# Kernel optimization log

Hardware: AMD Instinct MI355X
Metric: run time of the kernel (lower is better)

## Reference

```python
import jax, jax.numpy as jnp
import numpy as np

D_MODEL = 2048
EXPAND = 2
D_INNER = EXPAND * D_MODEL      # 4096
HEADDIM = 64
NHEADS = D_INNER // HEADDIM     # 64
D_STATE = 128
NGROUPS = 1
D_CONV = 4
CHUNK = 256
CONV_DIM = D_INNER + 2 * NGROUPS * D_STATE          # 4352
D_IN_PROJ = 2 * D_INNER + 2 * NGROUPS * D_STATE + NHEADS  # 8512
EPS = 1e-5


def setup_inputs() -> dict:
    key = jax.random.key(0)
    ks = jax.random.split(key, 8)
    B, L = 2, 2048
    u = jax.random.normal(ks[0], (B, L, D_MODEL), jnp.float32)
    W_in = jax.random.normal(ks[1], (D_IN_PROJ, D_MODEL), jnp.float32) / np.sqrt(D_MODEL)
    conv_w = jax.random.normal(ks[2], (CONV_DIM, D_CONV), jnp.float32) * 0.2
    conv_b = jax.random.normal(ks[3], (CONV_DIM,), jnp.float32) * 0.05
    # dt_bias initialized exactly as in the torch module
    dt = jnp.exp(jax.random.uniform(ks[4], (NHEADS,)) * (np.log(0.1) - np.log(0.001)) + np.log(0.001))
    dt = jnp.clip(dt, 1e-4)
    dt_bias = dt + jnp.log(-jnp.expm1(-dt))
    A_log = jnp.log(jax.random.uniform(ks[5], (NHEADS,), minval=1.0, maxval=16.0))
    D = jnp.ones((NHEADS,), jnp.float32)
    norm_w = jnp.ones((D_INNER,), jnp.float32)
    W_out = jax.random.normal(ks[6], (D_MODEL, D_INNER), jnp.float32) / np.sqrt(D_INNER)
    return dict(u=u, W_in=W_in, conv_w=conv_w, conv_b=conv_b, dt_bias=dt_bias,
                A_log=A_log, D=D, norm_w=norm_w, W_out=W_out)


def _segsum(x):
    # x: (..., l) -> (..., l, l) with out[i, j] = sum_{k=j+1..i} x[k] (lower-tri, -inf above)
    cs = jnp.cumsum(x, -1)
    seg = cs[..., :, None] - cs[..., None, :]
    l = x.shape[-1]
    mask = jnp.tril(jnp.ones((l, l), bool))
    return jnp.where(mask, seg, -jnp.inf)


def reference(u, W_in, conv_w, conv_b, dt_bias, A_log, D, norm_w, W_out):
    B, L, _ = u.shape
    zxbcdt = u @ W_in.T                                   # (B, L, 8512)
    z, xBC, dt_raw = jnp.split(zxbcdt, [D_INNER, D_INNER + CONV_DIM], axis=-1)
    # depthwise causal conv1d + SiLU (padding = d_conv-1, truncated to seqlen)
    xpad = jnp.pad(xBC, ((0, 0), (D_CONV - 1, 0), (0, 0)))
    xconv = conv_b + sum(xpad[:, w:w + L, :] * conv_w[:, w] for w in range(D_CONV))
    xBC = jax.nn.silu(xconv)
    x, Bm, Cm = jnp.split(xBC, [D_INNER, D_INNER + NGROUPS * D_STATE], axis=-1)
    x = x.reshape(B, L, NHEADS, HEADDIM)
    hpg = NHEADS // NGROUPS
    Bh = jnp.repeat(Bm.reshape(B, L, NGROUPS, D_STATE), hpg, axis=2)  # (B,L,H,N)
    Ch = jnp.repeat(Cm.reshape(B, L, NGROUPS, D_STATE), hpg, axis=2)
    dt = jax.nn.softplus(dt_raw + dt_bias)                # (B, L, H)
    A = -jnp.exp(A_log)                                   # (H,)
    nchunks = L // CHUNK
    def chunk(t):
        return t.reshape(B, nchunks, CHUNK, *t.shape[2:])
    xc, Bc, Cc, dtc = chunk(x), chunk(Bh), chunk(Ch), chunk(dt)
    xd = xc * dtc[..., None]                              # (B,C,Lc,H,P)
    dA = jnp.transpose(dtc * A, (0, 3, 1, 2))             # (B,H,C,Lc)
    A_cum = jnp.cumsum(dA, -1)
    Lmat = jnp.exp(_segsum(dA))                           # (B,H,C,Lc,Lc) lower-tri decays
    # intra-chunk (diagonal blocks)
    Y_diag = jnp.einsum('bclhn,bcshn,bhcls,bcshp->bclhp', Cc, Bc, Lmat, xd)
    # chunk end-states
    decay_states = jnp.exp(A_cum[..., -1:] - A_cum)       # (B,H,C,Lc)
    states = jnp.einsum('bclhn,bhcl,bclhp->bchpn', Bc, decay_states, xd)
    # inter-chunk recurrence over chunk states
    chunk_sums = jnp.pad(A_cum[..., -1], ((0, 0), (0, 0), (1, 0)))  # (B,H,C+1)
    decay_chunk = jnp.exp(_segsum(chunk_sums))            # (B,H,C+1,C+1)
    states_pad = jnp.concatenate([jnp.zeros_like(states[:, :1]), states], axis=1)
    new_states = jnp.einsum('bhzc,bchpn->bzhpn', decay_chunk, states_pad)
    prev_states = new_states[:, :-1]                      # (B,C,H,P,N)
    Y_off = jnp.einsum('bclhn,bchpn,bhcl->bclhp', Cc, prev_states, jnp.exp(A_cum))
    y = (Y_diag + Y_off).reshape(B, L, NHEADS, HEADDIM)
    y = y + x * D[None, None, :, None]                    # per-head D skip
    y = y.reshape(B, L, D_INNER)
    # gated RMSNorm (norm_before_gate=False): rmsnorm(y * silu(z)) * w
    yg = y * jax.nn.silu(z)
    var = jnp.mean(yg * yg, axis=-1, keepdims=True)
    y = yg * jax.lax.rsqrt(var + EPS) * norm_w
    return y @ W_out.T                                    # (B, L, d_model)
```

## Files before the change

### kernel.cpp

```cpp
#include <hip/hip_runtime.h>

#define D_MODEL   2048
#define D_INNER   4096
#define HEADDIM   64
#define NHEADS    64
#define D_STATE   128
#define CHUNK     256
#define CONV_DIM  4352
#define D_IN_PROJ 8512
#define BATCH     2
#define SEQ       2048
#define NCHUNK    8
#define NROWS     4096
#define EPSV      1e-5f
#define CG        (CONV_DIM / 8)

typedef __attribute__((ext_vector_type(8))) short bf16x8;
typedef __attribute__((ext_vector_type(8))) unsigned short u16x8;
typedef __attribute__((ext_vector_type(4))) float f32x4;

#define AS1 __attribute__((address_space(1)))
#define AS3 __attribute__((address_space(3)))

#define BAR() do { asm volatile("" ::: "memory"); __builtin_amdgcn_s_barrier(); asm volatile("" ::: "memory"); } while (0)

__device__ __forceinline__ unsigned short f2bf(float f) {
  unsigned int x = __float_as_uint(f);
  unsigned int r = (x + 0x7fffu + ((x >> 16) & 1u)) >> 16;
  return (unsigned short)r;
}
__device__ __forceinline__ float bf2f(unsigned short u) {
  return __uint_as_float((unsigned int)u << 16);
}

__global__ void k_sentinel(float* out) { if (threadIdx.x == 0) out[0] = 1.0e6f; }

__global__ void k_prep(const float* __restrict__ u, unsigned short* __restrict__ uhi, unsigned short* __restrict__ ulo,
                       const float* __restrict__ W, unsigned short* __restrict__ winb, unsigned short* __restrict__ whl,
                       const float* __restrict__ cw, const float* __restrict__ cb,
                       unsigned short* __restrict__ cwT, unsigned short* __restrict__ cbT) {
  const int b = blockIdx.x;
  const int t = threadIdx.x;
  if (b < 2048) {
    const long n4 = (long)NROWS * D_MODEL / 4;
    for (long i = (long)b * 256 + t; i < n4; i += 2048L * 256) {
      float4 v = ((const float4*)u)[i];
      ushort4 h, l;
      h.x = f2bf(v.x); l.x = f2bf(v.x - bf2f(h.x));
      h.y = f2bf(v.y); l.y = f2bf(v.y - bf2f(h.y));
      h.z = f2bf(v.z); l.z = f2bf(v.z - bf2f(h.z));
      h.w = f2bf(v.w); l.w = f2bf(v.w - bf2f(h.w));
      ((ushort4*)uhi)[i] = h;
      ((ushort4*)ulo)[i] = l;
    }
  } else if (b < 6144) {
    const long n4 = (long)D_IN_PROJ * D_MODEL / 4;
    for (long i = (long)(b - 2048) * 256 + t; i < n4; i += 4096L * 256) {
      float4 v = ((const float4*)W)[i];
      ushort4 o = make_ushort4(f2bf(v.x), f2bf(v.y), f2bf(v.z), f2bf(v.w));
      ((ushort4*)winb)[i] = o;
    }
  } else if (b < 6656) {
    long i = (long)(b - 6144) * 256 + t;
    float v = W[(size_t)8448 * D_MODEL + i];
    unsigned short h = f2bf(v);
    whl[i] = h;
    whl[(size_t)64 * D_MODEL + i] = f2bf(v - bf2f(h));
  } else {
    int i = (b - 6656) * 256 + t;
    if (i < CONV_DIM) {
#pragma unroll
      for (int w = 0; w < 4; ++w) cwT[w * CONV_DIM + i] = f2bf(cw[i * 4 + w]);
      cbT[i] = f2bf(cb[i]);
    }
  }
}

__global__ void k_f32_to_bf16_v4(const float* __restrict__ in, unsigned short* __restrict__ out, long n4) {
  long i = (long)blockIdx.x * blockDim.x + threadIdx.x;
  long stride = (long)gridDim.x * blockDim.x;
  for (; i < n4; i += stride) {
    float4 v = ((const float4*)in)[i];
    ushort4 o = make_ushort4(f2bf(v.x), f2bf(v.y), f2bf(v.z), f2bf(v.w));
    ((ushort4*)out)[i] = o;
  }
}

__global__ __launch_bounds__(256, 2) void k_dtm(const unsigned short* __restrict__ uhi,
                                                const unsigned short* __restrict__ ulo,
                                                const unsigned short* __restrict__ whl,
                                                float* __restrict__ PD) {
  __shared__ __align__(16) short lds[2][256 * 64];
  const int t = threadIdx.x;
  const int lane = t & 63;
  const int w = t >> 6;
  const int ks = (int)blockIdx.x & 3;
  const int m0 = ((int)blockIdx.x >> 2) * 64;
  const int kbase = ks * 512;

  f32x4 acc1[8], acc2[4];
#pragma unroll
  for (int j = 0; j < 8; ++j) { f32x4 z = {0.f, 0.f, 0.f, 0.f}; acc1[j] = z; }
#pragma unroll
  for (int j = 0; j < 4; ++j) { f32x4 z = {0.f, 0.f, 0.f, 0.f}; acc2[j] = z; }

  const int srow = t >> 3;
  const int schunk = (t & 7) ^ (srow & 7);
  const unsigned short* gU = uhi + (size_t)(m0 + srow) * D_MODEL + kbase + schunk * 8;
  const unsigned short* gL = ulo + (size_t)(m0 + srow) * D_MODEL + kbase + schunk * 8;
  const unsigned short* gW = whl + (size_t)srow * D_MODEL + kbase + schunk * 8;

  auto STAGE = [&](int buf, int kt) {
    char* d = (char*)&lds[buf][0] + t * 16;
#pragma unroll
    for (int ii = 0; ii < 2; ++ii)
      __builtin_amdgcn_global_load_lds((const AS1 void*)(gU + (size_t)ii * 32 * D_MODEL + (size_t)kt * 64),
                                       (AS3 void*)(d + ii * 4096), 16, 0, 0);
#pragma unroll
    for (int ii = 0; ii < 2; ++ii)
      __builtin_amdgcn_global_load_lds((const AS1 void*)(gL + (size_t)ii * 32 * D_MODEL + (size_t)kt * 64),
                                       (AS3 void*)(d + 8192 + ii * 4096), 16, 0, 0);
#pragma unroll
    for (int ii = 0; ii < 4; ++ii)
      __builtin_amdgcn_global_load_lds((const AS1 void*)(gW + (size_t)ii * 32 * D_MODEL + (size_t)kt * 64),
                                       (AS3 void*)(d + 16384 + ii * 4096), 16, 0, 0);
  };

  STAGE(0, 0);

  const int NT = 512 / 64;
  const int ar = w * 16 + (lane & 15);
  const int kof = (lane >> 4) * 8;
  const int rsw = (lane & 7) * 8;
  int cur = 0;
  for (int kt = 0; kt < NT; ++kt) {
    if (kt + 1 < NT) {
      STAGE(cur ^ 1, kt + 1);
      asm volatile("s_waitcnt vmcnt(8)" ::: "memory");
    } else {
      asm volatile("s_waitcnt vmcnt(0)" ::: "memory");
    }
    __builtin_amdgcn_s_barrier();
    asm volatile("" ::: "memory");
    const short* L = &lds[cur][0];
#pragma unroll
    for (int kk = 0; kk < 2; ++kk) {
      const int off = (kk * 32 + kof) ^ rsw;
      bf16x8 ah = *(const bf16x8*)(L + ar * 64 + off);
      bf16x8 al = *(const bf16x8*)(L + (64 + ar) * 64 + off);
#pragma unroll
      for (int j = 0; j < 8; ++j) {
        bf16x8 bj = *(const bf16x8*)(L + (128 + j * 16 + (lane & 15)) * 64 + off);
        acc1[j] = __builtin_amdgcn_mfma_f32_16x16x32_bf16(ah, bj, acc1[j], 0, 0, 0);
        if (j < 4) acc2[j] = __builtin_amdgcn_mfma_f32_16x16x32_bf16(al, bj, acc2[j], 0, 0, 0);
      }
    }
    asm volatile("" ::: "memory");
    __builtin_amdgcn_s_barrier();
    asm volatile("" ::: "memory");
    cur ^= 1;
  }

  const int crow = (lane >> 4) * 4;
  float* P = PD + (size_t)ks * BATCH * NHEADS * SEQ;
#pragma unroll
  for (int j = 0; j < 4; ++j) {
    int h = j * 16 + (lane & 15);
#pragma unroll
    for (int r = 0; r < 4; ++r) {
      int row = m0 + w * 16 + crow + r;
      float v = acc1[j][r] + acc1[j + 4][r] + acc2[j][r];
      P[(size_t)((row >> 11) * NHEADS + h) * SEQ + (row & 2047)] = v;
    }
  }
}

__global__ __launch_bounds__(256) void k_dtred(const float* __restrict__ PD, const float* __restrict__ dt_bias,
                                               const float* __restrict__ A_log,
                                               float* __restrict__ dt_t, float* __restrict__ A_cum) {
  const int bh = blockIdx.x;
  const int h = bh & 63;
  const int t = threadIdx.x;
  const float bias = dt_bias[h];
  const float A = -expf(A_log[h]);
  const size_t base = (size_t)bh * SEQ;
  const size_t pstride = (size_t)BATCH * NHEADS * SEQ;
  __shared__ float s[256];
  for (int c = 0; c < NCHUNK; ++c) {
    int l = c * CHUNK + t;
    float v = PD[base + l] + PD[pstride + base + l] + PD[2 * pstride + base + l] + PD[3 * pstride + base + l] + bias;
    float dtv = (v > 20.f) ? v : log1pf(expf(v));
    dt_t[base + l] = dtv;
    s[t] = dtv * A;
    __syncthreads();
    for (int off = 1; off < 256; off <<= 1) {
      float x = (t >= off) ? s[t - off] : 0.f;
      __syncthreads();
      s[t] += x;
      __syncthreads();
    }
    A_cum[((size_t)bh * NCHUNK + c) * CHUNK + t] = s[t];
    __syncthreads();
  }
}

__global__ __launch_bounds__(512, 2) void k_gemm8p(const unsigned short* __restrict__ A,
                                                   const unsigned short* __restrict__ B,
                                                   unsigned short* __restrict__ C, int M, int N, int K) {
  __shared__ __align__(16) short lds[2][32768];
  const int t = threadIdx.x;
  const int lane = t & 63;
  const int wid = t >> 6;
  const int wr = wid >> 2;
  const int wc = wid & 3;
  const int ntx = N / 256;
  const int nwg = (int)gridDim.x;
  const int bid = (int)blockIdx.x;
  const int swz = (bid & 7) * (nwg >> 3) + (bid >> 3);
  const int grp = ntx << 3;
  const int gid = swz / grp;
  const int rem = swz - gid * grp;
  const int m0 = ((gid << 3) + (rem & 7)) * 256;
  const int n0 = (rem >> 3) * 256;

  f32x4 acc[8][4];
#pragma unroll
  for (int i = 0; i < 8; ++i)
#pragma unroll
    for (int j = 0; j < 4; ++j) { f32x4 z = {0.f, 0.f, 0.f, 0.f}; acc[i][j] = z; }

  const int srow = t >> 3;
  const int schunk = (t & 7) ^ (srow & 7);
  const unsigned short* gA = A + (size_t)(m0 + srow) * K + schunk * 8;
  const unsigned short* gB = B + (size_t)(n0 + srow) * K + schunk * 8;

  auto STAGE_HALF = [&](int buf, int kt, int which) {
    const unsigned short* g = (which < 2 ? gA : gB) + (size_t)(which & 1) * 128 * K + (size_t)kt * 64;
    char* d = (char*)lds + buf * 65536 + which * 16384 + t * 16;
    __builtin_amdgcn_global_load_lds((const AS1 void*)g, (AS3 void*)d, 16, 0, 0);
    __builtin_amdgcn_global_load_lds((const AS1 void*)(g + (size_t)64 * K), (AS3 void*)(d + 8192), 16, 0, 0);
  };

  const int NT = K / 64;
  STAGE_HALF(0, 0, 0); STAGE_HALF(0, 0, 1); STAGE_HALF(0, 0, 2); STAGE_HALF(0, 0, 3);
  STAGE_HALF(1, 1, 2); STAGE_HALF(1, 1, 0); STAGE_HALF(1, 1, 1);
  asm volatile("s_waitcnt vmcnt(6)" ::: "memory");
  BAR();

  const int ar = wr * 128 + (lane & 15);
  const int br = wc * 64 + (lane & 15);
  const int kof = (lane >> 4) * 8;
  const int rsw = (lane & 7) * 8;

  for (int kt = 0; kt < NT; ++kt) {
    const int buf = kt & 1;
    const short* As = &lds[buf][0];
    const short* Bs = &lds[buf][16384];
    const bool s1 = (kt + 1 < NT);
    const bool s2 = (kt + 2 < NT);
    bf16x8 aLo[4][2], aHi[4][2], bLo[2][2], bHi[2][2];

#pragma unroll
    for (int i = 0; i < 4; ++i)
#pragma unroll
      for (int k = 0; k < 2; ++k) aLo[i][k] = *(const bf16x8*)(As + (ar + i * 16) * 64 + ((k * 32 + kof) ^ rsw));
#pragma unroll
    for (int j = 0; j < 2; ++j)
#pragma unroll
      for (int k = 0; k < 2; ++k) bLo[j][k] = *(const bf16x8*)(Bs + (br + j * 16) * 64 + ((k * 32 + kof) ^ rsw));
    if (s1) STAGE_HALF(buf ^ 1, kt + 1, 3);
    BAR();
    __builtin_amdgcn_s_setprio(1);
#pragma unroll
    for (int k = 0; k < 2; ++k)
#pragma unroll
      for (int i = 0; i < 4; ++i)
#pragma unroll
        for (int j = 0; j < 2; ++j)
          acc[i][j] = __builtin_amdgcn_mfma_f32_16x16x32_bf16(aLo[i][k], bLo[j][k], acc[i][j], 0, 0, 0);
    __builtin_amdgcn_s_setprio(0);
    BAR();

#pragma unroll
    for (int j = 0; j < 2; ++j)
#pragma unroll
      for (int k = 0; k < 2; ++k) bHi[j][k] = *(const bf16x8*)(Bs + (br + (j + 2) * 16) * 64 + ((k * 32 + kof) ^ rsw));
    BAR();
    __builtin_amdgcn_s_setprio(1);
#pragma unroll
    for (int k = 0; k < 2; ++k)
#pragma unroll
      for (int i = 0; i < 4; ++i)
#pragma unroll
        for (int j = 0; j < 2; ++j)
          acc[i][j + 2] = __builtin_amdgcn_mfma_f32_16x16x32_bf16(aLo[i][k], bHi[j][k], acc[i][j + 2], 0, 0, 0);
    __builtin_amdgcn_s_setprio(0);
    BAR();

#pragma unroll
    for (int i = 0; i < 4; ++i)
#pragma unroll
      for (int k = 0; k < 2; ++k) aHi[i][k] = *(const bf16x8*)(As + (ar + (i + 4) * 16) * 64 + ((k * 32 + kof) ^ rsw));
    if (s2) STAGE_HALF(buf, kt + 2, 2);
    BAR();
    __builtin_amdgcn_s_setprio(1);
#pragma unroll
    for (int k = 0; k < 2; ++k)
#pragma unroll
      for (int i = 0; i < 4; ++i)
#pragma unroll
        for (int j = 0; j < 2; ++j)
          acc[i + 4][j] = __builtin_amdgcn_mfma_f32_16x16x32_bf16(aHi[i][k], bLo[j][k], acc[i + 4][j], 0, 0, 0);
    __builtin_amdgcn_s_setprio(0);
    BAR();

    if (s2) { STAGE_HALF(buf, kt + 2, 0); STAGE_HALF(buf, kt + 2, 1); }
    if (s2) { asm volatile("s_waitcnt vmcnt(6)" ::: "memory"); }
    else    { asm volatile("s_waitcnt vmcnt(0)" ::: "memory"); }
    BAR();
    __builtin_amdgcn_s_setprio(1);
#pragma unroll
    for (int k = 0; k < 2; ++k)
#pragma unroll
      for (int i = 0; i < 4; ++i)
#pragma unroll
        for (int j = 0; j < 2; ++j)
          acc[i + 4][j + 2] = __builtin_amdgcn_mfma_f32_16x16x32_bf16(aHi[i][k], bHi[j][k], acc[i + 4][j + 2], 0, 0, 0);
    __builtin_amdgcn_s_setprio(0);
    BAR();
  }

  const int crow = (lane >> 4) * 4;
  const int ccol = lane & 15;
#pragma unroll
  for (int i = 0; i < 8; ++i)
#pragma unroll
    for (int j = 0; j < 4; ++j) {
      size_t base = (size_t)(m0 + wr * 128 + i * 16 + crow) * N + (n0 + wc * 64 + j * 16 + ccol);
#pragma unroll
      for (int r = 0; r < 4; ++r) C[base + (size_t)r * N] = f2bf(acc[i][j][r]);
    }
}

template <int BF16OUT>
__global__ __launch_bounds__(256, 2) void k_gemm128(const unsigned short* __restrict__ A,
                                                    const unsigned short* __restrict__ B,
                                                    void* __restrict__ Cv, int M, int N, int K) {
  constexpr int BK = 64;
  __shared__ __align__(16) short lds[2][256 * BK];
  const int t = threadIdx.x;
  const int lane = t & 63;
  const int wid = t >> 6;
  const int wr = wid >> 1;
  const int wc = wid & 1;
  const int ntx = N / 128;
  const int nwg = (int)gridDim.x;
  const int bid = (int)blockIdx.x;
  const int swz = (bid & 7) * (nwg >> 3) + (bid >> 3);
  const int grp = ntx << 3;
  const int gid = swz / grp;
  const int rem = swz - gid * grp;
  const int m0 = ((gid << 3) + (rem & 7)) * 128;
  const int n0 = (rem >> 3) * 128;

  f32x4 acc[4][4];
#pragma unroll
  for (int i = 0; i < 4; ++i)
#pragma unroll
    for (int j = 0; j < 4; ++j) { f32x4 z = {0.f, 0.f, 0.f, 0.f}; acc[i][j] = z; }

  const int srow = t >> 3;
  const int schunk = (t & 7) ^ (srow & 7);
  const unsigned short* gA = A + (size_t)(m0 + srow) * K + schunk * 8;
  const unsigned short* gB = B + (size_t)(n0 + srow) * K + schunk * 8;

  auto STAGE = [&](int buf, int kt) {
    char* dA = (char*)&lds[buf][0] + t * 16;
    char* dB = (char*)&lds[buf][128 * BK] + t * 16;
#pragma unroll
    for (int ii = 0; ii < 4; ++ii)
      __builtin_amdgcn_global_load_lds((const AS1 void*)(gA + (size_t)ii * 32 * K + kt * BK),
                                       (AS3 void*)(dA + ii * 4096), 16, 0, 0);
#pragma unroll
    for (int ii = 0; ii < 4; ++ii)
      __builtin_amdgcn_global_load_lds((const AS1 void*)(gB + (size_t)ii * 32 * K + kt * BK),
                                       (AS3 void*)(dB + ii * 4096), 16, 0, 0);
  };

  STAGE(0, 0);

  const int NT = K / BK;
  const int ar = wr * 64 + (lane & 15);
  const int br = wc * 64 + (lane & 15);
  const int kof = (lane >> 4) * 8;
  const int rsw = (lane & 7) * 8;
  int cur = 0;
  for (int kt = 0; kt < NT; ++kt) {
    if (kt + 1 < NT) {
      STAGE(cur ^ 1, kt + 1);
      asm volatile("s_waitcnt vmcnt(8)" ::: "memory");
    } else {
      asm volatile("s_waitcnt vmcnt(0)" ::: "memory");
    }
    __builtin_amdgcn_s_barrier();
    asm volatile("" ::: "memory");
    const short* As = &lds[cur][0];
    const short* Bs = &lds[cur][128 * BK];
#pragma unroll
    for (int kk = 0; kk < 2; ++kk) {
      bf16x8 bfr[4];
#pragma unroll
      for (int j = 0; j < 4; ++j)
        bfr[j] = *(const bf16x8*)(Bs + (br + j * 16) * BK + ((kk * 32 + kof) ^ rsw));
#pragma unroll
      for (int i = 0; i < 4; ++i) {
        bf16x8 af = *(const bf16x8*)(As + (ar + i * 16) * BK + ((kk * 32 + kof) ^ rsw));
#pragma unroll
        for (int j = 0; j < 4; ++j)
          acc[i][j] = __builtin_amdgcn_mfma_f32_16x16x32_bf16(af, bfr[j], acc[i][j], 0, 0, 0);
      }
    }
    asm volatile("" ::: "memory");
    __builtin_amdgcn_s_barrier();
    asm volatile("" ::: "memory");
    cur ^= 1;
  }

  const int crow = (lane >> 4) * 4;
  const int ccol = lane & 15;
#pragma unroll
  for (int i = 0; i < 4; ++i)
#pragma unroll
    for (int j = 0; j < 4; ++j) {
      size_t base = (size_t)(m0 + wr * 64 + i * 16 + crow) * N + (n0 + wc * 64 + j * 16 + ccol);
      if (BF16OUT) {
        unsigned short* C = (unsigned short*)Cv;
#pragma unroll
        for (int r = 0; r < 4; ++r) C[base + (size_t)r * N] = f2bf(acc[i][j][r]);
      } else {
        float* C = (float*)Cv;
#pragma unroll
        for (int r = 0; r < 4; ++r) C[base + (size_t)r * N] = acc[i][j][r];
      }
    }
}

__global__ __launch_bounds__(256) void k_conv_silu(const unsigned short* __restrict__ xb,
                                                   const unsigned short* __restrict__ wT,
                                                   const unsigned short* __restrict__ bT,
                                                   unsigned short* __restrict__ out) {
  long idx = (long)blockIdx.x * blockDim.x + threadIdx.x;
  if (idx >= (long)(NROWS / 4) * CG) return;
  int c8 = (int)(idx % CG);
  long rq = idx / CG;
  int l0 = (int)((rq & (SEQ / 4 - 1)) * 4);
  long brow = (rq >> 9) * (long)SEQ;
  int ch0 = c8 * 8;

  u16x8 wv[4];
#pragma unroll
  for (int w = 0; w < 4; ++w) wv[w] = *(const u16x8*)(wT + w * CONV_DIM + ch0);
  u16x8 bv = *(const u16x8*)(bT + ch0);

  u16x8 xr[7];
#pragma unroll
  for (int i = 0; i < 7; ++i) {
    int ls = l0 - 3 + i;
    if (ls >= 0) xr[i] = *(const u16x8*)(xb + (brow + ls) * (long)CONV_DIM + ch0);
    else { u16x8 z = {0, 0, 0, 0, 0, 0, 0, 0}; xr[i] = z; }
  }

#pragma unroll
  for (int r = 0; r < 4; ++r) {
    float acc[8];
#pragma unroll
    for (int e = 0; e < 8; ++e) acc[e] = bf2f(bv[e]);
#pragma unroll
    for (int w = 0; w < 4; ++w)
#pragma unroll
      for (int e = 0; e < 8; ++e) acc[e] += bf2f(xr[r + w][e]) * bf2f(wv[w][e]);
    u16x8 o;
#pragma unroll
    for (int e = 0; e < 8; ++e) o[e] = f2bf(acc[e] / (1.f + expf(-acc[e])));
    *(u16x8*)(out + (brow + l0 + r) * (long)CONV_DIM + ch0) = o;
  }
}

__global__ __launch_bounds__(256) void k_cbtt(const unsigned short* __restrict__ xbc, unsigned short* __restrict__ cbt_t) {
  const int bid = blockIdx.x;
  const int sp = bid & 3;
  const int bc = bid >> 2;
  const int b = bc >> 3, c = bc & 7;
  const int t = threadIdx.x;
  const int lane = t & 63;
  const int w = t >> 6;
  const int g = lane >> 4;
  __shared__ unsigned short Cs[256][72];
  __shared__ unsigned short Bs2[64][72];
  const long rowbase = (long)b * SEQ + c * CHUNK;
  f32x4 acc[4][4];
#pragma unroll
  for (int i = 0; i < 4; ++i)
#pragma unroll
    for (int j = 0; j < 4; ++j) { f32x4 z = {0.f, 0.f, 0.f, 0.f}; acc[i][j] = z; }

  for (int np = 0; np < 2; ++np) {
    __syncthreads();
    for (int i = t; i < 256 * 16; i += 256) {
      int row = i >> 4, c4 = (i & 15) * 4;
      ushort4 v = *(const ushort4*)(xbc + (rowbase + row) * (long)CONV_DIM + D_INNER + D_STATE + np * 64 + c4);
      *(ushort4*)&Cs[row][c4] = v;
    }
    for (int i = t; i < 64 * 16; i += 256) {
      int row = i >> 4, c4 = (i & 15) * 4;
      ushort4 v = *(const ushort4*)(xbc + (rowbase + sp * 64 + row) * (long)CONV_DIM + D_INNER + np * 64 + c4);
      *(ushort4*)&Bs2[row][c4] = v;
    }
    __syncthreads();
#pragma unroll
    for (int ks = 0; ks < 2; ++ks) {
      const int kofs = ks * 32 + g * 8;
      bf16x8 af[4], bfr[4];
#pragma unroll
      for (int i = 0; i < 4; ++i) af[i] = *(const bf16x8*)&Cs[w * 64 + i * 16 + (lane & 15)][kofs];
#pragma unroll
      for (int j = 0; j < 4; ++j) bfr[j] = *(const bf16x8*)&Bs2[j * 16 + (lane & 15)][kofs];
#pragma unroll
      for (int i = 0; i < 4; ++i)
#pragma unroll
        for (int j = 0; j < 4; ++j)
          acc[i][j] = __builtin_amdgcn_mfma_f32_16x16x32_bf16(af[i], bfr[j], acc[i][j], 0, 0, 0);
    }
  }
  unsigned short* ob = cbt_t + (long)bc * CHUNK * CHUNK;
#pragma unroll
  for (int i = 0; i < 4; ++i)
#pragma unroll
    for (int j = 0; j < 4; ++j) {
      int l0 = w * 64 + i * 16 + g * 4;
      int s = sp * 64 + j * 16 + (lane & 15);
#pragma unroll
      for (int r = 0; r < 4; ++r) ob[(long)(l0 + r) * CHUNK + s] = f2bf(acc[i][j][r]);
    }
}

__global__ __launch_bounds__(256) void k_states(const unsigned short* __restrict__ xbc, const float* __restrict__ dt_t,
                                                const float* __restrict__ A_cum, float* __restrict__ states) {
  const int bid = blockIdx.x;
  const int h = bid & 63;
  const int bc = bid >> 6;
  const int b = bc >> 3, c = bc & 7;
  const int t = threadIdx.x;
  const int lane = t & 63;
  const int w = t >> 6;
  const int g = lane >> 4;
  __shared__ unsigned short BT[128][72];
  __shared__ unsigned short WXT[64][72];
  __shared__ float csL[256], dtL[256];
  const long rowbase = (long)b * SEQ + c * CHUNK;
  const long bh8 = ((long)(b * NHEADS + h)) * NCHUNK + c;
  const float* acum = A_cum + bh8 * CHUNK;
  if (t < 256) { csL[t] = acum[t]; dtL[t] = dt_t[((size_t)(b * NHEADS + h)) * SEQ + c * CHUNK + t]; }
  float cs_last = acum[255];
  f32x4 acc[2][4];
#pragma unroll
  for (int i = 0; i < 2; ++i)
#pragma unroll
    for (int j = 0; j < 4; ++j) { f32x4 z = {0.f, 0.f, 0.f, 0.f}; acc[i][j] = z; }

  for (int lp = 0; lp < 4; ++lp) {
    __syncthreads();
    for (int i = t; i < 64 * 32; i += 256) {
      int l = i >> 5, n4 = (i & 31) * 4;
      ushort4 v = *(const ushort4*)(xbc + (rowbase + lp * 64 + l) * (long)CONV_DIM + D_INNER + n4);
      BT[n4 + 0][l] = v.x; BT[n4 + 1][l] = v.y; BT[n4 + 2][l] = v.z; BT[n4 + 3][l] = v.w;
    }
    for (int i = t; i < 64 * 16; i += 256) {
      int l = i >> 4, p4 = (i & 15) * 4;
      int lg = lp * 64 + l;
      float wgt = expf(cs_last - csL[lg]) * dtL[lg];
      ushort4 v = *(const ushort4*)(xbc + (rowbase + lg) * (long)CONV_DIM + h * HEADDIM + p4);
      WXT[p4 + 0][l] = f2bf(bf2f(v.x) * wgt);
      WXT[p4 + 1][l] = f2bf(bf2f(v.y) * wgt);
      WXT[p4 + 2][l] = f2bf(bf2f(v.z) * wgt);
      WXT[p4 + 3][l] = f2bf(bf2f(v.w) * wgt);
    }
    __syncthreads();
#pragma unroll
    for (int ks = 0; ks < 2; ++ks) {
      const int kofs = ks * 32 + g * 8;
      bf16x8 am[2], bp[4];
#pragma unroll
      for (int i = 0; i < 2; ++i) am[i] = *(const bf16x8*)&BT[w * 32 + i * 16 + (lane & 15)][kofs];
#pragma unroll
      for (int j = 0; j < 4; ++j) bp[j] = *(const bf16x8*)&WXT[j * 16 + (lane & 15)][kofs];
#pragma unroll
      for (int i = 0; i < 2; ++i)
#pragma unroll
        for (int j = 0; j < 4; ++j)
          acc[i][j] = __builtin_amdgcn_mfma_f32_16x16x32_bf16(am[i], bp[j], acc[i][j], 0, 0, 0);
    }
  }
  float* sp = states + ((long)bc * NHEADS + h) * (D_STATE * HEADDIM);
#pragma unroll
  for (int i = 0; i < 2; ++i)
#pragma unroll
    for (int j = 0; j < 4; ++j) {
      int n0 = w * 32 + i * 16 + g * 4;
      int p = j * 16 + (lane & 15);
#pragma unroll
      for (int r = 0; r < 4; ++r) sp[(long)(n0 + r) * HEADDIM + p] = acc[i][j][r];
    }
}

__global__ void k_scan(const float* __restrict__ states, const float* __restrict__ A_cum, unsigned short* __restrict__ psb) {
  long idx = (long)blockIdx.x * blockDim.x + threadIdx.x;
  if (idx >= (long)BATCH * NHEADS * D_STATE * HEADDIM) return;
  int p = idx & 63;
  int n = (int)((idx >> 6) & 127);
  long bh = idx >> 13;
  int h = (int)(bh & 63);
  int b = (int)(bh >> 6);
  float S = 0.f;
  for (int c = 0; c < NCHUNK; ++c) {
    long soff = (((long)(b * NCHUNK + c) * NHEADS + h) * (D_STATE * HEADDIM)) + (long)n * HEADDIM + p;
    psb[soff] = f2bf(S);
    float decay = expf(A_cum[(bh * NCHUNK + c) * CHUNK + 255]);
    S = S * decay + states[soff];
  }
}

__global__ __launch_bounds__(256) void k_y(const unsigned short* __restrict__ xbc, const float* __restrict__ dt_t,
                                           const float* __restrict__ A_cum, const unsigned short* __restrict__ cbt_t,
                                           const unsigned short* __restrict__ psb, const float* __restrict__ Dp,
                                           unsigned short* __restrict__ y) {
  const int bid = blockIdx.x;
  const int h = bid & 63;
  const int bc = bid >> 6;
  const int b = bc >> 3, c = bc & 7;
  const int t = threadIdx.x;
  const int lane = t & 63;
  const int w = t >> 6;
  const int g = lane >> 4;
  __shared__ unsigned short Abuf[256][72];
  __shared__ unsigned short Bbuf[64][72];
  __shared__ float csL[256], dtL[256], expL[256];
  const long rowbase = (long)b * SEQ + c * CHUNK;
  const long bh8 = ((long)(b * NHEADS + h)) * NCHUNK + c;
  const float* acum = A_cum + bh8 * CHUNK;
  if (t < 256) {
    float cv = acum[t];
    csL[t] = cv;
    expL[t] = expf(cv);
    dtL[t] = dt_t[((size_t)(b * NHEADS + h)) * SEQ + c * CHUNK + t];
  }
  f32x4 acc[4][4];
#pragma unroll
  for (int i = 0; i < 4; ++i)
#pragma unroll
    for (int j = 0; j < 4; ++j) { f32x4 z = {0.f, 0.f, 0.f, 0.f}; acc[i][j] = z; }

  const unsigned short* psbase = psb + ((long)bc * NHEADS + h) * (D_STATE * HEADDIM);
  for (int np = 0; np < 2; ++np) {
    __syncthreads();
    for (int i = t; i < 256 * 16; i += 256) {
      int row = i >> 4, c4 = (i & 15) * 4;
      float el = expL[row];
      ushort4 v = *(const ushort4*)(xbc + (rowbase + row) * (long)CONV_DIM + D_INNER + D_STATE + np * 64 + c4);
      ushort4 o = make_ushort4(f2bf(bf2f(v.x) * el), f2bf(bf2f(v.y) * el), f2bf(bf2f(v.z) * el), f2bf(bf2f(v.w) * el));
      *(ushort4*)&Abuf[row][c4] = o;
    }
    for (int i = t; i < 64 * 16; i += 256) {
      int n = i >> 4, p4 = (i & 15) * 4;
      ushort4 v = *(const ushort4*)(psbase + (long)(np * 64 + n) * HEADDIM + p4);
      Bbuf[p4 + 0][n] = v.x; Bbuf[p4 + 1][n] = v.y; Bbuf[p4 + 2][n] = v.z; Bbuf[p4 + 3][n] = v.w;
    }
    __syncthreads();
#pragma unroll
    for (int ks = 0; ks < 2; ++ks) {
      const int kofs = ks * 32 + g * 8;
      bf16x8 af[4], bfr[4];
#pragma unroll
      for (int i = 0; i < 4; ++i) af[i] = *(const bf16x8*)&Abuf[w * 64 + i * 16 + (lane & 15)][kofs];
#pragma unroll
      for (int j = 0; j < 4; ++j) bfr[j] = *(const bf16x8*)&Bbuf[j * 16 + (lane & 15)][kofs];
#pragma unroll
      for (int i = 0; i < 4; ++i)
#pragma unroll
        for (int j = 0; j < 4; ++j)
          acc[i][j] = __builtin_amdgcn_mfma_f32_16x16x32_bf16(af[i], bfr[j], acc[i][j], 0, 0, 0);
    }
  }

  const unsigned short* cbtb = cbt_t + (long)bc * CHUNK * CHUNK;
  for (int sp = 0; sp < 4; ++sp) {
    __syncthreads();
    for (int i = t; i < 64 * 8; i += 256) {
      int s = i >> 3, p0 = (i & 7) * 8;
      u16x8 v = *(const u16x8*)(xbc + (rowbase + sp * 64 + s) * (long)CONV_DIM + h * HEADDIM + p0);
#pragma unroll
      for (int e = 0; e < 8; ++e) Bbuf[p0 + e][s] = v[e];
    }
    __syncthreads();
    if (sp > w) continue;
#pragma unroll
    for (int ks = 0; ks < 2; ++ks) {
      const int kofs = ks * 32 + g * 8;
      bf16x8 bfr[4];
#pragma unroll
      for (int j = 0; j < 4; ++j) bfr[j] = *(const bf16x8*)&Bbuf[j * 16 + (lane & 15)][kofs];
      const int sbase = sp * 64 + ks * 32 + g * 8;
#pragma unroll
      for (int i = 0; i < 4; ++i) {
        if (sp == w && ks * 32 > i * 16 + 15) continue;
        const int l = w * 64 + i * 16 + (lane & 15);
        u16x8 cv = *(const u16x8*)(cbtb + (long)l * CHUNK + sbase);
        const float cl = csL[l];
        bf16x8 af;
#pragma unroll
        for (int e = 0; e < 8; ++e) {
          int s = sbase + e;
          float val = (s <= l) ? bf2f(cv[e]) * expf(cl - csL[s]) * dtL[s] : 0.f;
          af[e] = (short)f2bf(val);
        }
#pragma unroll
        for (int j = 0; j < 4; ++j)
          acc[i][j] = __builtin_amdgcn_mfma_f32_16x16x32_bf16(af, bfr[j], acc[i][j], 0, 0, 0);
      }
    }
  }

  const float Dh = Dp[h];
#pragma unroll
  for (int i = 0; i < 4; ++i) {
    int l0 = w * 64 + i * 16 + g * 4;
#pragma unroll
    for (int r = 0; r < 4; ++r) {
      long grow = rowbase + l0 + r;
      const unsigned short* xrow = xbc + grow * (long)CONV_DIM + h * HEADDIM;
      unsigned short* yrow = y + grow * (long)D_INNER + h * HEADDIM;
#pragma unroll
      for (int j = 0; j < 4; ++j) {
        int p = j * 16 + (lane & 15);
        yrow[p] = f2bf(acc[i][j][r] + bf2f(xrow[p]) * Dh);
      }
    }
  }
}

__global__ __launch_bounds__(256) void k_norm(unsigned short* yz, const unsigned short* __restrict__ zb,
                                              const float* __restrict__ norm_w, unsigned short* out) {
  const int row = blockIdx.x;
  const int t = threadIdx.x;
  const unsigned short* yr = yz + (size_t)row * D_INNER;
  const unsigned short* zr = zb + (size_t)row * D_INNER;
  float yv[16];
  float ss = 0.f;
#pragma unroll
  for (int j = 0; j < 4; ++j) {
    int e = (t + j * 256) * 4;
    ushort4 yy = *(const ushort4*)(yr + e);
    ushort4 zz = *(const ushort4*)(zr + e);
    float z0 = bf2f(zz.x), z1 = bf2f(zz.y), z2 = bf2f(zz.z), z3 = bf2f(zz.w);
    float g0 = bf2f(yy.x) * z0 / (1.f + expf(-z0));
    float g1 = bf2f(yy.y) * z1 / (1.f + expf(-z1));
    float g2 = bf2f(yy.z) * z2 / (1.f + expf(-z2));
    float g3 = bf2f(yy.w) * z3 / (1.f + expf(-z3));
    ss += g0 * g0 + g1 * g1 + g2 * g2 + g3 * g3;
    yv[j * 4 + 0] = g0; yv[j * 4 + 1] = g1; yv[j * 4 + 2] = g2; yv[j * 4 + 3] = g3;
  }
#pragma unroll
  for (int off = 32; off > 0; off >>= 1) ss += __shfl_xor(ss, off);
  __shared__ float red[4];
  if ((t & 63) == 0) red[t >> 6] = ss;
  __syncthreads();
  float tot = red[0] + red[1] + red[2] + red[3];
  float scale = rsqrtf(tot / (float)D_INNER + EPSV);
  unsigned short* orow = out + (size_t)row * D_INNER;
#pragma unroll
  for (int j = 0; j < 4; ++j) {
    int e = (t + j * 256) * 4;
    float4 w = *(const float4*)(norm_w + e);
    ushort4 o = make_ushort4(f2bf(yv[j * 4 + 0] * scale * w.x), f2bf(yv[j * 4 + 1] * scale * w.y),
                             f2bf(yv[j * 4 + 2] * scale * w.z), f2bf(yv[j * 4 + 3] * scale * w.w));
    *(ushort4*)(orow + e) = o;
  }
}

extern "C" void kernel_launch(void* const* d_in, const int* in_sizes, int n_in,
                              void* d_out, int out_size, void* d_ws, size_t ws_size,
                              hipStream_t stream) {
  const float* u       = (const float*)d_in[0];
  const float* W_in    = (const float*)d_in[1];
  const float* conv_w  = (const float*)d_in[2];
  const float* conv_b  = (const float*)d_in[3];
  const float* dt_bias = (const float*)d_in[4];
  const float* A_log   = (const float*)d_in[5];
  const float* Dp      = (const float*)d_in[6];
  const float* norm_w  = (const float*)d_in[7];
  const float* W_out   = (const float*)d_in[8];
  float* out = (float*)d_out;

  char* ws = (char*)d_ws;
  size_t off = 0;
  auto alloc = [&](size_t bytes) { char* p = ws + off; off += (bytes + 255) & ~(size_t)255; return p; };
  unsigned short* ub   = (unsigned short*)alloc((size_t)NROWS * D_MODEL * 2);
  unsigned short* winb = (unsigned short*)alloc((size_t)D_IN_PROJ * D_MODEL * 2);
  unsigned short* zb   = (unsigned short*)alloc((size_t)NROWS * D_INNER * 2);
  unsigned short* xb   = (unsigned short*)alloc((size_t)NROWS * CONV_DIM * 2);
  unsigned short* xbcb = (unsigned short*)alloc((size_t)NROWS * CONV_DIM * 2);
  float* dtt  = (float*)alloc((size_t)BATCH * NHEADS * SEQ * 4);
  float* acum = (float*)alloc((size_t)BATCH * NHEADS * NCHUNK * CHUNK * 4);
  unsigned short* cwT = (unsigned short*)alloc((size_t)4 * CONV_DIM * 2);
  unsigned short* cbT = (unsigned short*)alloc((size_t)CONV_DIM * 2);
  unsigned short* whl = (unsigned short*)alloc((size_t)128 * D_MODEL * 2);
  float* PD = (float*)alloc((size_t)4 * BATCH * NHEADS * SEQ * 4);
  unsigned short* wob = ub;
  unsigned short* cbt = winb;
  unsigned short* psb = winb + (size_t)BATCH * NCHUNK * CHUNK * CHUNK + 1024;
  unsigned short* ulob = xbcb;
  unsigned short* yb = xb;
  float* states = (float*)d_out;

  if (off > ws_size) {
    k_sentinel<<<1, 64, 0, stream>>>(out);
    return;
  }

  k_prep<<<6673, 256, 0, stream>>>(u, ub, ulob, W_in, winb, whl, conv_w, conv_b, cwT, cbT);
  k_gemm8p<<<(NROWS / 256) * (D_INNER / 256), 512, 0, stream>>>(ub, winb, zb, NROWS, D_INNER, D_MODEL);
  k_gemm128<1><<<(NROWS / 128) * (CONV_DIM / 128), 256, 0, stream>>>(ub, winb + (size_t)D_INNER * D_MODEL, xb, NROWS, CONV_DIM, D_MODEL);
  k_dtm<<<256, 256, 0, stream>>>(ub, ulob, whl, PD);
  k_dtred<<<BATCH * NHEADS, 256, 0, stream>>>(PD, dt_bias, A_log, dtt, acum);
  k_conv_silu<<<(int)(((long)(NROWS / 4) * CG + 255) / 256), 256, 0, stream>>>(xb, cwT, cbT, xbcb);
  k_cbtt<<<BATCH * NCHUNK * 4, 256, 0, stream>>>(xbcb, cbt);
  k_states<<<BATCH * NCHUNK * NHEADS, 256, 0, stream>>>(xbcb, dtt, acum, states);
  k_scan<<<(BATCH * NHEADS * D_STATE * HEADDIM + 255) / 256, 256, 0, stream>>>(states, acum, psb);
  k_y<<<BATCH * NCHUNK * NHEADS, 256, 0, stream>>>(xbcb, dtt, acum, cbt, psb, Dp, yb);
  k_norm<<<NROWS, 256, 0, stream>>>(yb, zb, norm_w, yb);
  k_f32_to_bf16_v4<<<2048, 256, 0, stream>>>(W_out, wob, (long)D_MODEL * D_INNER / 4);
  k_gemm128<0><<<(NROWS / 128) * (D_MODEL / 128), 256, 0, stream>>>(yb, wob, out, NROWS, D_MODEL, D_INNER);
}
```

Baseline: 478.5 us.

## Swizzle LDS tiles, tile CB^T layout, interleave row ownership, use fast exp

Replaces expf with __expf across several kernels. Stores the CB^T matrix in a 16x8 tiled layout so the diagonal-block kernel reads it with contiguous vector loads. XOR-swizzles the transposed LDS tiles in the states and output kernels to avoid bank conflicts. The output kernel now interleaves row blocks across waves so the causal work is spread evenly, and its C*prev_state pass is split into four K-steps of 32 with smaller LDS. Fast exp may slightly change numerical accuracy.

```diff
diff --git a/kernel.cpp b/kernel.cpp
--- a/kernel.cpp
+++ b/kernel.cpp
@@ -182,7 +182,7 @@
   const int h = bh & 63;
   const int t = threadIdx.x;
   const float bias = dt_bias[h];
-  const float A = -expf(A_log[h]);
+  const float A = -__expf(A_log[h]);
   const size_t base = (size_t)bh * SEQ;
   const size_t pstride = (size_t)BATCH * NHEADS * SEQ;
   __shared__ float s[256];
@@ -481,7 +481,7 @@
       for (int e = 0; e < 8; ++e) acc[e] += bf2f(xr[r + w][e]) * bf2f(wv[w][e]);
     u16x8 o;
 #pragma unroll
-    for (int e = 0; e < 8; ++e) o[e] = f2bf(acc[e] / (1.f + expf(-acc[e])));
+    for (int e = 0; e < 8; ++e) o[e] = f2bf(acc[e] / (1.f + __expf(-acc[e])));
     *(u16x8*)(out + (brow + l0 + r) * (long)CONV_DIM + ch0) = o;
   }
 }
@@ -540,7 +540,10 @@
       int l0 = w * 64 + i * 16 + g * 4;
       int s = sp * 64 + j * 16 + (lane & 15);
 #pragma unroll
-      for (int r = 0; r < 4; ++r) ob[(long)(l0 + r) * CHUNK + s] = f2bf(acc[i][j][r]);
+      for (int r = 0; r < 4; ++r) {
+        int l = l0 + r;
+        ob[((long)(l >> 4) * 32 + (s >> 3)) * 128 + (l & 15) * 8 + (s & 7)] = f2bf(acc[i][j][r]);
+      }
     }
 }
 
@@ -572,18 +575,20 @@
     __syncthreads();
     for (int i = t; i < 64 * 32; i += 256) {
       int l = i >> 5, n4 = (i & 31) * 4;
+      int sw = ((n4 >> 3) & 7) << 3;
       ushort4 v = *(const ushort4*)(xbc + (rowbase + lp * 64 + l) * (long)CONV_DIM + D_INNER + n4);
-      BT[n4 + 0][l] = v.x; BT[n4 + 1][l] = v.y; BT[n4 + 2][l] = v.z; BT[n4 + 3][l] = v.w;
+      BT[n4 + 0][l ^ sw] = v.x; BT[n4 + 1][l ^ sw] = v.y; BT[n4 + 2][l ^ sw] = v.z; BT[n4 + 3][l ^ sw] = v.w;
     }
     for (int i = t; i < 64 * 16; i += 256) {
       int l = i >> 4, p4 = (i & 15) * 4;
+      int sw = ((p4 >> 3) & 7) << 3;
       int lg = lp * 64 + l;
-      float wgt = expf(cs_last - csL[lg]) * dtL[lg];
+      float wgt = __expf(cs_last - csL[lg]) * dtL[lg];
       ushort4 v = *(const ushort4*)(xbc + (rowbase + lg) * (long)CONV_DIM + h * HEADDIM + p4);
-      WXT[p4 + 0][l] = f2bf(bf2f(v.x) * wgt);
-      WXT[p4 + 1][l] = f2bf(bf2f(v.y) * wgt);
-      WXT[p4 + 2][l] = f2bf(bf2f(v.z) * wgt);
-      WXT[p4 + 3][l] = f2bf(bf2f(v.w) * wgt);
+      WXT[p4 + 0][l ^ sw] = f2bf(bf2f(v.x) * wgt);
+      WXT[p4 + 1][l ^ sw] = f2bf(bf2f(v.y) * wgt);
+      WXT[p4 + 2][l ^ sw] = f2bf(bf2f(v.z) * wgt);
+      WXT[p4 + 3][l ^ sw] = f2bf(bf2f(v.w) * wgt);
     }
     __syncthreads();
 #pragma unroll
@@ -591,9 +596,15 @@
       const int kofs = ks * 32 + g * 8;
       bf16x8 am[2], bp[4];
 #pragma unroll
-      for (int i = 0; i < 2; ++i) am[i] = *(const bf16x8*)&BT[w * 32 + i * 16 + (lane & 15)][kofs];
-#pragma unroll
-      for (int j = 0; j < 4; ++j) bp[j] = *(const bf16x8*)&WXT[j * 16 + (lane & 15)][kofs];
+      for (int i = 0; i < 2; ++i) {
+        int row = w * 32 + i * 16 + (lane & 15);
+        am[i] = *(const bf16x8*)&BT[row][kofs ^ (((row >> 3) & 7) << 3)];
+      }
+#pragma unroll
+      for (int j = 0; j < 4; ++j) {
+        int row = j * 16 + (lane & 15);
+        bp[j] = *(const bf16x8*)&WXT[row][kofs ^ (((row >> 3) & 7) << 3)];
+      }
 #pragma unroll
       for (int i = 0; i < 2; ++i)
 #pragma unroll
@@ -625,7 +636,7 @@
   for (int c = 0; c < NCHUNK; ++c) {
     long soff = (((long)(b * NCHUNK + c) * NHEADS + h) * (D_STATE * HEADDIM)) + (long)n * HEADDIM + p;
     psb[soff] = f2bf(S);
-    float decay = expf(A_cum[(bh * NCHUNK + c) * CHUNK + 255]);
+    float decay = __expf(A_cum[(bh * NCHUNK + c) * CHUNK + 255]);
     S = S * decay + states[soff];
   }
 }
@@ -642,7 +653,7 @@
   const int lane = t & 63;
   const int w = t >> 6;
   const int g = lane >> 4;
-  __shared__ unsigned short Abuf[256][72];
+  __shared__ unsigned short Abuf[256][56];
   __shared__ unsigned short Bbuf[64][72];
   __shared__ float csL[256], dtL[256], expL[256];
   const long rowbase = (long)b * SEQ + c * CHUNK;
@@ -651,7 +662,7 @@
   if (t < 256) {
     float cv = acum[t];
     csL[t] = cv;
-    expL[t] = expf(cv);
+    expL[t] = __expf(cv);
     dtL[t] = dt_t[((size_t)(b * NHEADS + h)) * SEQ + c * CHUNK + t];
   }
   f32x4 acc[4][4];
@@ -661,66 +672,71 @@
     for (int j = 0; j < 4; ++j) { f32x4 z = {0.f, 0.f, 0.f, 0.f}; acc[i][j] = z; }
 
   const unsigned short* psbase = psb + ((long)bc * NHEADS + h) * (D_STATE * HEADDIM);
-  for (int np = 0; np < 2; ++np) {
-    __syncthreads();
-    for (int i = t; i < 256 * 16; i += 256) {
-      int row = i >> 4, c4 = (i & 15) * 4;
+  for (int np = 0; np < 4; ++np) {
+    __syncthreads();
+    for (int i = t; i < 256 * 8; i += 256) {
+      int row = i >> 3, c4 = (i & 7) * 4;
       float el = expL[row];
-      ushort4 v = *(const ushort4*)(xbc + (rowbase + row) * (long)CONV_DIM + D_INNER + D_STATE + np * 64 + c4);
+      ushort4 v = *(const ushort4*)(xbc + (rowbase + row) * (long)CONV_DIM + D_INNER + D_STATE + np * 32 + c4);
       ushort4 o = make_ushort4(f2bf(bf2f(v.x) * el), f2bf(bf2f(v.y) * el), f2bf(bf2f(v.z) * el), f2bf(bf2f(v.w) * el));
       *(ushort4*)&Abuf[row][c4] = o;
     }
-    for (int i = t; i < 64 * 16; i += 256) {
-      int n = i >> 4, p4 = (i & 15) * 4;
-      ushort4 v = *(const ushort4*)(psbase + (long)(np * 64 + n) * HEADDIM + p4);
-      Bbuf[p4 + 0][n] = v.x; Bbuf[p4 + 1][n] = v.y; Bbuf[p4 + 2][n] = v.z; Bbuf[p4 + 3][n] = v.w;
-    }
-    __syncthreads();
-#pragma unroll
-    for (int ks = 0; ks < 2; ++ks) {
-      const int kofs = ks * 32 + g * 8;
-      bf16x8 af[4], bfr[4];
-#pragma unroll
-      for (int i = 0; i < 4; ++i) af[i] = *(const bf16x8*)&Abuf[w * 64 + i * 16 + (lane & 15)][kofs];
-#pragma unroll
-      for (int j = 0; j < 4; ++j) bfr[j] = *(const bf16x8*)&Bbuf[j * 16 + (lane & 15)][kofs];
-#pragma unroll
-      for (int i = 0; i < 4; ++i)
-#pragma unroll
-        for (int j = 0; j < 4; ++j)
-          acc[i][j] = __builtin_amdgcn_mfma_f32_16x16x32_bf16(af[i], bfr[j], acc[i][j], 0, 0, 0);
+    for (int i = t; i < 512; i += 256) {
+      int nl = i >> 4, p4 = (i & 15) * 4;
+      int sw = ((p4 >> 3) & 7) << 3;
+      ushort4 v = *(const ushort4*)(psbase + (long)(np * 32 + nl) * HEADDIM + p4);
+      Bbuf[p4 + 0][nl ^ sw] = v.x; Bbuf[p4 + 1][nl ^ sw] = v.y;
+      Bbuf[p4 + 2][nl ^ sw] = v.z; Bbuf[p4 + 3][nl ^ sw] = v.w;
+    }
+    __syncthreads();
+    bf16x8 bfr[4];
+#pragma unroll
+    for (int j = 0; j < 4; ++j) {
+      int row = j * 16 + (lane & 15);
+      bfr[j] = *(const bf16x8*)&Bbuf[row][(g * 8) ^ (((row >> 3) & 7) << 3)];
+    }
+#pragma unroll
+    for (int i = 0; i < 4; ++i) {
+      bf16x8 af = *(const bf16x8*)&Abuf[(i * 4 + w) * 16 + (lane & 15)][g * 8];
+#pragma unroll
+      for (int j = 0; j < 4; ++j)
+        acc[i][j] = __builtin_amdgcn_mfma_f32_16x16x32_bf16(af, bfr[j], acc[i][j], 0, 0, 0);
     }
   }
 
   const unsigned short* cbtb = cbt_t + (long)bc * CHUNK * CHUNK;
   for (int sp = 0; sp < 4; ++sp) {
     __syncthreads();
-    for (int i = t; i < 64 * 8; i += 256) {
+    for (int i = t; i < 512; i += 256) {
       int s = i >> 3, p0 = (i & 7) * 8;
+      int sw = ((p0 >> 3) & 7) << 3;
       u16x8 v = *(const u16x8*)(xbc + (rowbase + sp * 64 + s) * (long)CONV_DIM + h * HEADDIM + p0);
 #pragma unroll
-      for (int e = 0; e < 8; ++e) Bbuf[p0 + e][s] = v[e];
-    }
-    __syncthreads();
-    if (sp > w) continue;
+      for (int e = 0; e < 8; ++e) Bbuf[p0 + e][s ^ sw] = v[e];
+    }
+    __syncthreads();
 #pragma unroll
     for (int ks = 0; ks < 2; ++ks) {
-      const int kofs = ks * 32 + g * 8;
+      const int sb0 = sp * 64 + ks * 32;
       bf16x8 bfr[4];
 #pragma unroll
-      for (int j = 0; j < 4; ++j) bfr[j] = *(const bf16x8*)&Bbuf[j * 16 + (lane & 15)][kofs];
-      const int sbase = sp * 64 + ks * 32 + g * 8;
+      for (int j = 0; j < 4; ++j) {
+        int row = j * 16 + (lane & 15);
+        bfr[j] = *(const bf16x8*)&Bbuf[row][(ks * 32 + g * 8) ^ (((row >> 3) & 7) << 3)];
+      }
+      const int sbase = sb0 + g * 8;
 #pragma unroll
       for (int i = 0; i < 4; ++i) {
-        if (sp == w && ks * 32 > i * 16 + 15) continue;
-        const int l = w * 64 + i * 16 + (lane & 15);
-        u16x8 cv = *(const u16x8*)(cbtb + (long)l * CHUNK + sbase);
+        const int L0 = (i * 4 + w) * 16;
+        if (sb0 > L0 + 15) continue;
+        const int l = L0 + (lane & 15);
+        u16x8 cv = *(const u16x8*)(cbtb + ((long)(L0 >> 4) * 32 + (sbase >> 3)) * 128 + (l & 15) * 8);
         const float cl = csL[l];
         bf16x8 af;
 #pragma unroll
         for (int e = 0; e < 8; ++e) {
           int s = sbase + e;
-          float val = (s <= l) ? bf2f(cv[e]) * expf(cl - csL[s]) * dtL[s] : 0.f;
+          float val = (s <= l) ? bf2f(cv[e]) * __expf(cl - csL[s]) * dtL[s] : 0.f;
           af[e] = (short)f2bf(val);
         }
 #pragma unroll
@@ -733,7 +749,7 @@
   const float Dh = Dp[h];
 #pragma unroll
   for (int i = 0; i < 4; ++i) {
-    int l0 = w * 64 + i * 16 + g * 4;
+    int l0 = (i * 4 + w) * 16 + g * 4;
 #pragma unroll
     for (int r = 0; r < 4; ++r) {
       long grow = rowbase + l0 + r;
@@ -762,10 +778,10 @@
     ushort4 yy = *(const ushort4*)(yr + e);
     ushort4 zz = *(const ushort4*)(zr + e);
     float z0 = bf2f(zz.x), z1 = bf2f(zz.y), z2 = bf2f(zz.z), z3 = bf2f(zz.w);
-    float g0 = bf2f(yy.x) * z0 / (1.f + expf(-z0));
-    float g1 = bf2f(yy.y) * z1 / (1.f + expf(-z1));
-    float g2 = bf2f(yy.z) * z2 / (1.f + expf(-z2));
-    float g3 = bf2f(yy.w) * z3 / (1.f + expf(-z3));
+    float g0 = bf2f(yy.x) * z0 / (1.f + __expf(-z0));
+    float g1 = bf2f(yy.y) * z1 / (1.f + __expf(-z1));
+    float g2 = bf2f(yy.z) * z2 / (1.f + __expf(-z2));
+    float g3 = bf2f(yy.w) * z3 / (1.f + __expf(-z3));
     ss += g0 * g0 + g1 * g1 + g2 * g2 + g3 * g3;
     yv[j * 4 + 0] = g0; yv[j * 4 + 1] = g1; yv[j * 4 + 2] = g2; yv[j * 4 + 3] = g3;
   }
```

Result: faster. 438.3 us, median of 2 (-8.4%).
